# Kernel tuning notes

Measured on AMD Instinct MI355X. Metric: run time of the kernel, lower is better.

## Reference

```python
import jax, jax.numpy as jnp
import numpy as np

B, S, E, H = 2, 2048, 4096, 32
D = E // H  # head_dim = 128
MAX_SEQ = 2048


def precompute_freqs(dim, end, theta=10000.0):
    # Faithful to the torch source, including its operator precedence:
    # freqs = 1.0 / (theta ** arange(0, dim, 2)[:dim//2].float() / dim)
    # i.e. 1.0 / ((theta ** exps) / dim); overflows to inf in fp32 -> freq 0.
    exps = jnp.arange(0, dim, 2, dtype=jnp.float32)[: dim // 2]
    freqs = 1.0 / (jnp.power(jnp.float32(theta), exps) / jnp.float32(dim))
    t = jnp.arange(end, dtype=jnp.float32)
    f = jnp.outer(t, freqs)  # [end, dim//2]
    return jnp.cos(f), jnp.sin(f)


def apply_rope(x, cos, sin, pos):
    # x: [B,H,S,D]; cos/sin: [max_seq, dim//2]; pos: [B,S]
    c = cos[pos][:, None]  # [B,1,S,f]
    s = sin[pos][:, None]
    xr = x.reshape(*x.shape[:-1], -1, 2)  # [B,H,S,D/2,2]
    x1, x2 = xr[..., 0], xr[..., 1]
    if x1.shape[-1] > c.shape[-1]:
        rep = x1.shape[-1] // c.shape[-1]  # repeat_interleave factor
        c = jnp.repeat(c, rep, axis=-1)
        s = jnp.repeat(s, rep, axis=-1)
    out = jnp.stack([x1 * c - x2 * s, x1 * s + x2 * c], axis=-1)
    return out.reshape(x.shape)


def setup_inputs() -> dict:
    key = jax.random.key(0)
    kx, kq, kk, kv, ko = jax.random.split(key, 5)
    x = jax.random.normal(kx, (B, S, E), jnp.float32)
    scale = 0.02
    Wq = jax.random.normal(kq, (E, E), jnp.float32) * scale
    Wk = jax.random.normal(kk, (E, E), jnp.float32) * scale
    Wv = jax.random.normal(kv, (E, E), jnp.float32) * scale
    Wo = jax.random.normal(ko, (E, E), jnp.float32) * scale
    z = jnp.zeros((E,), jnp.float32)
    return {"x": x, "Wq": Wq, "bq": z, "Wk": Wk, "bk": z, "Wv": Wv, "bv": z, "Wo": Wo, "bo": z}


def reference(x, Wq, bq, Wk, bk, Wv, bv, Wo, bo):
    cos, sin = precompute_freqs(H, MAX_SEQ)  # note: dim = n_heads, as in source
    pos = jnp.broadcast_to(jnp.arange(S)[None, :], (B, S))  # no offset, S <= max
    # QKV projections (torch Linear: x @ W.T + b)
    q = (x @ Wq.T + bq).reshape(B, S, H, D).transpose(0, 2, 1, 3)  # [B,H,S,D]
    k = (x @ Wk.T + bk).reshape(B, S, H, D).transpose(0, 2, 1, 3)
    v = (x @ Wv.T + bv).reshape(B, S, H, D).transpose(0, 2, 1, 3)
    q = apply_rope(q, cos, sin, pos)
    k = apply_rope(k, cos, sin, pos)
    # SDPA with mask=None (non-causal, full attention)
    scores = jnp.einsum("bhqd,bhkd->bhqk", q, k) / np.float32(np.sqrt(D))
    att = jax.nn.softmax(scores, axis=-1)
    out = jnp.einsum("bhqk,bhkd->bhqd", att, v)
    out = out.transpose(0, 2, 1, 3).reshape(B, S, E)
    return out @ Wo.T + bo
```

## Files before the change

kernel.cpp:

```cpp
#include <hip/hip_runtime.h>
#include <math.h>

typedef _Float16 half8 __attribute__((ext_vector_type(8)));
typedef _Float16 half4 __attribute__((ext_vector_type(4)));
typedef __fp16 fp16x2 __attribute__((ext_vector_type(2)));
typedef float f32x4 __attribute__((ext_vector_type(4)));
typedef unsigned uint4v __attribute__((ext_vector_type(4)));

struct FreqT { float f[16]; };

__device__ __forceinline__ f32x4 mfma16(half8 a, half8 b, f32x4 c) {
  return __builtin_amdgcn_mfma_f32_16x16x32_f16(a, b, c, 0, 0, 0);
}

__device__ __forceinline__ void gload_lds16(const void* g, void* l) {
  __builtin_amdgcn_global_load_lds(
      (const __attribute__((address_space(1))) void*)g,
      (__attribute__((address_space(3))) void*)l, 16, 0, 0);
}

__device__ __forceinline__ unsigned pk_f16(float p0, float p1) {
  fp16x2 h = __builtin_amdgcn_cvt_pkrtz(p0, p1);
  return __builtin_bit_cast(unsigned, h);
}

#define S_BARRIER() __builtin_amdgcn_s_barrier()
#define WAIT_LGKM0() asm volatile("s_waitcnt lgkmcnt(0)" ::: "memory")
#define WAIT_VM8() asm volatile("s_waitcnt vmcnt(8)" ::: "memory")
#define WAIT_VM4() asm volatile("s_waitcnt vmcnt(4)" ::: "memory")
#define WAIT_VM0() asm volatile("s_waitcnt vmcnt(0)" ::: "memory")

__global__ __launch_bounds__(256)
void cast_f32_f16(const float* __restrict__ in, _Float16* __restrict__ out, long n8) {
  long i = (long)blockIdx.x * blockDim.x + threadIdx.x;
  if (i >= n8) return;
  float4 a = ((const float4*)in)[2 * i];
  float4 b = ((const float4*)in)[2 * i + 1];
  half8 v;
  v[0] = (_Float16)a.x; v[1] = (_Float16)a.y; v[2] = (_Float16)a.z; v[3] = (_Float16)a.w;
  v[4] = (_Float16)b.x; v[5] = (_Float16)b.y; v[6] = (_Float16)b.z; v[7] = (_Float16)b.w;
  ((half8*)out)[i] = v;
}

#define GBM 256
#define GBN 256
#define GBK 64

template <typename OutT>
__global__ __launch_bounds__(512, 2)
void gemm256(const _Float16* __restrict__ A, const _Float16* __restrict__ W,
             const float* __restrict__ bias, OutT* __restrict__ C,
             int M, int N, int K) {
  __shared__ __align__(16) _Float16 lds[4][GBM * GBK];

  int nwg = gridDim.x;
  int bid = blockIdx.x;
  int cpx = nwg >> 3;
  int swz = (bid & 7) * cpx + (bid >> 3);
  int ntn = N / GBN;
  int m0 = (swz / ntn) * GBM, n0 = (swz % ntn) * GBN;

  int tid = threadIdx.x, lane = tid & 63, w = tid >> 6;
  int wm = w >> 2, wn = w & 3;
  int g = lane >> 4, lc = lane & 15;

  int r8 = w * 8 + (lane >> 3);
  int cs = (((lane & 7) ^ (lane >> 3)) << 3);
  const _Float16* gA = A + (size_t)(m0 + r8) * K + cs;
  const _Float16* gB = W + (size_t)(n0 + r8) * K + cs;

#define STAGE(bi, k0) do {                                            \
    _Float16* la_ = &lds[(bi) * 2][0] + w * 512;                      \
    _Float16* lb_ = &lds[(bi) * 2 + 1][0] + w * 512;                  \
    _Pragma("unroll")                                                 \
    for (int i_ = 0; i_ < 4; ++i_) {                                  \
      gload_lds16(gA + (size_t)(i_ * 64) * K + (k0), la_ + i_ * 4096);\
      gload_lds16(gB + (size_t)(i_ * 64) * K + (k0), lb_ + i_ * 4096);\
    } } while (0)

  int aOff[8], bOff[4];
#pragma unroll
  for (int mf = 0; mf < 8; ++mf) aOff[mf] = (wm * 128 + mf * 16 + lc) * 64;
#pragma unroll
  for (int nf = 0; nf < 4; ++nf) bOff[nf] = (wn * 64 + nf * 16 + lc) * 64;
  int co0 = (((0 * 4 + g) ^ (lc & 7)) << 3);
  int co1 = (((1 * 4 + g) ^ (lc & 7)) << 3);

  half8 a0[8], a1[8], b0[4], b1[4];
  f32x4 acc[8][4] = {};

#define LOAD_SET0(bi) do {                                            \
    const _Float16* lA_ = &lds[(bi) * 2][0];                          \
    const _Float16* lB_ = &lds[(bi) * 2 + 1][0];                      \
    _Pragma("unroll")                                                 \
    for (int mf = 0; mf < 4; ++mf) {                                  \
      a0[mf * 2 + 0] = *(const half8*)&lA_[aOff[mf] + co0];           \
      a0[mf * 2 + 1] = *(const half8*)&lA_[aOff[mf] + co1];           \
    }                                                                 \
    _Pragma("unroll")                                                 \
    for (int nf = 0; nf < 2; ++nf) {                                  \
      b0[nf * 2 + 0] = *(const half8*)&lB_[bOff[nf] + co0];           \
      b0[nf * 2 + 1] = *(const half8*)&lB_[bOff[nf] + co1];           \
    } } while (0)

#define LOAD_SET1(bi) do {                                            \
    const _Float16* lA_ = &lds[(bi) * 2][0];                          \
    const _Float16* lB_ = &lds[(bi) * 2 + 1][0];                      \
    _Pragma("unroll")                                                 \
    for (int mf = 0; mf < 4; ++mf) {                                  \
      a1[mf * 2 + 0] = *(const half8*)&lA_[aOff[mf + 4] + co0];       \
      a1[mf * 2 + 1] = *(const half8*)&lA_[aOff[mf + 4] + co1];       \
    }                                                                 \
    _Pragma("unroll")                                                 \
    for (int nf = 0; nf < 2; ++nf) {                                  \
      b1[nf * 2 + 0] = *(const half8*)&lB_[bOff[nf + 2] + co0];       \
      b1[nf * 2 + 1] = *(const half8*)&lB_[bOff[nf + 2] + co1];       \
    } } while (0)

#define MFMA_Q(mq, nq, ar, br) do {                                   \
    __builtin_amdgcn_s_setprio(1);                                    \
    _Pragma("unroll")                                                 \
    for (int mf = 0; mf < 4; ++mf)                                    \
      _Pragma("unroll")                                               \
      for (int nf = 0; nf < 2; ++nf)                                  \
        _Pragma("unroll")                                             \
        for (int kk = 0; kk < 2; ++kk)                                \
          acc[(mq) * 4 + mf][(nq) * 2 + nf] =                         \
              mfma16(ar[mf * 2 + kk], br[nf * 2 + kk],                \
                     acc[(mq) * 4 + mf][(nq) * 2 + nf]);              \
    __builtin_amdgcn_s_setprio(0); } while (0)

  const int NT = K >> 6;

  STAGE(0, 0);
  STAGE(1, GBK);
  WAIT_VM8();
  S_BARRIER();
  LOAD_SET0(0);

  for (int t = 0; t < NT - 2; ++t) {
    int cur = t & 1;
    LOAD_SET1(cur);
    MFMA_Q(0, 0, a0, b0);
    MFMA_Q(0, 1, a0, b1);
    WAIT_LGKM0();
    S_BARRIER();
    STAGE(cur, (t + 2) << 6);
    MFMA_Q(1, 1, a1, b1);
    MFMA_Q(1, 0, a1, b0);
    WAIT_VM8();
    S_BARRIER();
    LOAD_SET0(cur ^ 1);
  }
  {
    int cur = (NT - 2) & 1;
    LOAD_SET1(cur);
    MFMA_Q(0, 0, a0, b0);
    MFMA_Q(0, 1, a0, b1);
    MFMA_Q(1, 1, a1, b1);
    MFMA_Q(1, 0, a1, b0);
    WAIT_VM0();
    S_BARRIER();
    LOAD_SET0(cur ^ 1);
  }
  {
    LOAD_SET1((NT - 1) & 1);
    MFMA_Q(0, 0, a0, b0);
    MFMA_Q(0, 1, a0, b1);
    MFMA_Q(1, 1, a1, b1);
    MFMA_Q(1, 0, a1, b0);
  }

  int crow = m0 + wm * 128 + g * 4;
  int ccol = n0 + wn * 64 + lc;
#pragma unroll
  for (int nf = 0; nf < 4; ++nf) {
    float bv = bias[ccol + nf * 16];
#pragma unroll
    for (int mf = 0; mf < 8; ++mf)
#pragma unroll
      for (int j = 0; j < 4; ++j)
        C[(size_t)(crow + mf * 16 + j) * N + ccol + nf * 16] =
            (OutT)(acc[mf][nf][j] + bv);
  }
#undef STAGE
#undef LOAD_SET0
#undef LOAD_SET1
#undef MFMA_Q
}

__global__ __launch_bounds__(256)
void rope_kernel(_Float16* __restrict__ x, FreqT ft, int Sn, int E, long n8) {
  long i = (long)blockIdx.x * blockDim.x + threadIdx.x;
  if (i >= n8) return;
  int epr = E / 8;
  int e8 = (int)(i % epr);
  int s = (int)((i / epr) % Sn);
  int fj = e8 & 15;
  float fr = ft.f[fj];
  float ang = (float)s * fr;
  float sv, cv;
  sincosf(ang, &sv, &cv);
  half8 v = ((const half8*)x)[i];
  half8 o;
#pragma unroll
  for (int p = 0; p < 4; ++p) {
    float x1 = (float)v[2 * p], x2 = (float)v[2 * p + 1];
    o[2 * p] = (_Float16)(x1 * cv - x2 * sv);
    o[2 * p + 1] = (_Float16)(x1 * sv + x2 * cv);
  }
  ((half8*)x)[i] = o;
}

__global__ __launch_bounds__(256)
void transpose_v(const _Float16* __restrict__ v, _Float16* __restrict__ vt,
                 int Hn, int Sn) {
  const int D = 128;
  const int E = Hn * D;
  __shared__ _Float16 t[64][130];
  int spb = Sn / 64;
  int bid = blockIdx.x;
  int s0 = (bid % spb) * 64;
  int bh = bid / spb;
  int b = bh / Hn, h = bh % Hn;
  int tid = threadIdx.x;
  int r = tid >> 2, dc = (tid & 3) * 32;
  const _Float16* src = v + (size_t)(b * Sn + s0 + r) * E + h * D + dc;
#pragma unroll
  for (int i = 0; i < 4; ++i) {
    half8 x = *(const half8*)(src + i * 8);
#pragma unroll
    for (int k = 0; k < 4; ++k) {
      _Float16 a0 = x[2 * k], a1 = x[2 * k + 1];
      t[r][dc + i * 8 + 2 * k] = a0;
      t[r][dc + i * 8 + 2 * k + 1] = a1;
    }
  }
  __syncthreads();
  int d = tid >> 1, sh = (tid & 1) * 32;
  half8 ov[4];
#pragma unroll
  for (int c = 0; c < 4; ++c)
#pragma unroll
    for (int j = 0; j < 8; ++j)
      ov[c][j] = t[sh + c * 8 + j][d];
  _Float16* dst = vt + ((size_t)bh * D + d) * Sn + s0 + sh;
#pragma unroll
  for (int c = 0; c < 4; ++c)
    *(half8*)(dst + c * 8) = ov[c];
}

#define QB 128
#define KB 64

__global__ __launch_bounds__(256, 3)
void flash_attn(const _Float16* __restrict__ qg, const _Float16* __restrict__ kg,
                const _Float16* __restrict__ vt, _Float16* __restrict__ og,
                int Bn, int Hn, int Sn) {
  const int D = 128;
  const int E = Hn * D;

  __shared__ _Float16 Ksh[2][KB * 128];
  __shared__ _Float16 Vsh[D * KB];
  __shared__ float sm[4][32];

  int qtiles = Sn / QB;
  int bid = blockIdx.x;
  int bh = bid / qtiles, qt = bid % qtiles;
  int b = bh / Hn, h = bh % Hn;

  int tid = threadIdx.x, lane = tid & 63, w = tid >> 6;
  int g = lane >> 4, lc = lane & 15;
  int lc7 = lc & 7;

  const size_t headoff = ((size_t)b * Sn) * E + (size_t)h * D;
  const _Float16* qp = qg + headoff;
  const _Float16* kp = kg + headoff;
  const _Float16* vtp = vt + (size_t)(b * Hn + h) * D * Sn;

  int q0 = qt * QB + w * 32;
  half8 aq[2][4];
#pragma unroll
  for (int mf = 0; mf < 2; ++mf)
#pragma unroll
    for (int kf = 0; kf < 4; ++kf)
      aq[mf][kf] = *(const half8*)(qp + (size_t)(q0 + mf * 16 + lc) * E + kf * 32 + g * 8);

  float mrun[2] = {-1e30f, -1e30f}, lpart[2] = {0.f, 0.f};
  f32x4 o[2][8] = {};

  const float scale = 0.08838834764831845f;

  int krow = 4 * w + (lane >> 4);
  int kcol = ((lane & 15) ^ (krow & 7)) * 8;
  const _Float16* gK = kp + (size_t)krow * E + kcol;
  int vrow = w * 32 + (lane >> 3);
  int vcol = ((lane & 7) ^ (vrow & 7)) * 8;
  const _Float16* gV = vtp + (size_t)vrow * Sn + vcol;

  float* smw = sm[w];

  const int NT = Sn / KB;

  {
    _Float16* lK = Ksh[0] + w * 512;
#pragma unroll
    for (int i = 0; i < 4; ++i)
      gload_lds16(gK + (size_t)(16 * i) * E, lK + i * 2048);
  }
  WAIT_VM0();
  S_BARRIER();

  for (int t = 0; t < NT; ++t) {
    int c = t & 1;
    {
      _Float16* lV = Vsh + w * 2048;
#pragma unroll
      for (int p = 0; p < 4; ++p)
        gload_lds16(gV + (size_t)(p * 8) * Sn + t * KB, lV + p * 512);
    }
    if (t + 1 < NT) {
      _Float16* lK = Ksh[c ^ 1] + w * 512;
#pragma unroll
      for (int i = 0; i < 4; ++i)
        gload_lds16(gK + (size_t)((t + 1) * KB + 16 * i) * E, lK + i * 2048);
    }

    f32x4 st[2][4] = {};
    {
      const _Float16* Kc = Ksh[c];
      __builtin_amdgcn_s_setprio(1);
#pragma unroll
      for (int kf = 0; kf < 4; ++kf) {
        half8 bk[4];
#pragma unroll
        for (int nf = 0; nf < 4; ++nf)
          bk[nf] = *(const half8*)&Kc[(nf * 16 + lc) * 128 + (((kf * 4 + g) ^ lc7) << 3)];
#pragma unroll
        for (int nf = 0; nf < 4; ++nf)
#pragma unroll
          for (int mf = 0; mf < 2; ++mf)
            st[mf][nf] = mfma16(bk[nf], aq[mf][kf], st[mf][nf]);
      }
      __builtin_amdgcn_s_setprio(0);
    }

    bool resc[2];
#pragma unroll
    for (int mf = 0; mf < 2; ++mf) {
      f32x4 m4 = st[mf][0];
#pragma unroll
      for (int nf = 1; nf < 4; ++nf)
#pragma unroll
        for (int j = 0; j < 4; ++j) m4[j] = fmaxf(m4[j], st[mf][nf][j]);
      float mx = fmaxf(fmaxf(m4[0], m4[1]), fmaxf(m4[2], m4[3]));
      mx = fmaxf(mx, __shfl_xor(mx, 16));
      mx = fmaxf(mx, __shfl_xor(mx, 32));
      mx *= scale;
      resc[mf] = __any(mx > mrun[mf] + 8.f);
      if (resc[mf]) {
        float mnew = fmaxf(mrun[mf], mx);
        float r = __expf(mrun[mf] - mnew);
        mrun[mf] = mnew;
        lpart[mf] *= r;
        if (g == 0) smw[mf * 16 + lc] = r;
      }
    }
#pragma unroll
    for (int mf = 0; mf < 2; ++mf)
      if (resc[mf]) {
        f32x4 rv = *(const f32x4*)&smw[mf * 16 + g * 4];
#pragma unroll
        for (int df = 0; df < 8; ++df)
#pragma unroll
          for (int j = 0; j < 4; ++j) o[mf][df][j] *= rv[j];
      }

    half8 pa[2][2];
#pragma unroll
    for (int mf = 0; mf < 2; ++mf) {
      unsigned pk[4][2];
#pragma unroll
      for (int nf = 0; nf < 4; ++nf)
#pragma unroll
        for (int jj = 0; jj < 2; ++jj) {
          float p0 = __expf(st[mf][nf][2 * jj] * scale - mrun[mf]);
          float p1 = __expf(st[mf][nf][2 * jj + 1] * scale - mrun[mf]);
          lpart[mf] += p0 + p1;
          pk[nf][jj] = pk_f16(p0, p1);
        }
#pragma unroll
      for (int kk = 0; kk < 2; ++kk) {
        unsigned A0 = pk[2 * kk][0], B0 = pk[2 * kk + 1][0];
        asm("v_permlane32_swap_b32 %0, %1" : "+v"(A0), "+v"(B0));
        asm("v_permlane16_swap_b32 %0, %1" : "+v"(A0), "+v"(B0));
        unsigned A1 = pk[2 * kk][1], B1 = pk[2 * kk + 1][1];
        asm("v_permlane32_swap_b32 %0, %1" : "+v"(A1), "+v"(B1));
        asm("v_permlane16_swap_b32 %0, %1" : "+v"(A1), "+v"(B1));
        uint4v pv;
        pv[0] = A0; pv[1] = A1; pv[2] = B0; pv[3] = B1;
        pa[mf][kk] = __builtin_bit_cast(half8, pv);
      }
    }

    if (t + 1 < NT) { WAIT_VM4(); } else { WAIT_VM0(); }
    S_BARRIER();

    __builtin_amdgcn_s_setprio(1);
#pragma unroll
    for (int kk = 0; kk < 2; ++kk) {
      int csw = ((kk * 4 + g) ^ lc7) << 3;
#pragma unroll
      for (int df = 0; df < 8; ++df) {
        half8 bv = *(const half8*)&Vsh[(df * 16 + lc) * 64 + csw];
        o[0][df] = mfma16(pa[0][kk], bv, o[0][df]);
        o[1][df] = mfma16(pa[1][kk], bv, o[1][df]);
      }
    }
    __builtin_amdgcn_s_setprio(0);

    if (t + 1 < NT) {
      WAIT_VM0();
      S_BARRIER();
    }
  }

#pragma unroll
  for (int mf = 0; mf < 2; ++mf) {
    float l = lpart[mf];
    l += __shfl_xor(l, 16);
    l += __shfl_xor(l, 32);
    if (g == 0) smw[mf * 16 + lc] = 1.0f / l;
  }
  _Float16* op = og + headoff;
#pragma unroll
  for (int mf = 0; mf < 2; ++mf) {
    f32x4 li = *(const f32x4*)&smw[mf * 16 + g * 4];
#pragma unroll
    for (int j = 0; j < 4; ++j) {
      int row = q0 + mf * 16 + g * 4 + j;
#pragma unroll
      for (int df = 0; df < 8; ++df)
        op[(size_t)row * E + df * 16 + lc] = (_Float16)(o[mf][df][j] * li[j]);
    }
  }
}

extern "C" void kernel_launch(void* const* d_in, const int* in_sizes, int n_in,
                              void* d_out, int out_size, void* d_ws, size_t ws_size,
                              hipStream_t stream) {
  const float* x  = (const float*)d_in[0];
  const float* Wq = (const float*)d_in[1];
  const float* bq = (const float*)d_in[2];
  const float* Wk = (const float*)d_in[3];
  const float* bk = (const float*)d_in[4];
  const float* Wv = (const float*)d_in[5];
  const float* bv = (const float*)d_in[6];
  const float* Wo = (const float*)d_in[7];
  const float* bo = (const float*)d_in[8];

  const int E = in_sizes[2];
  const int M = in_sizes[0] / E;
  const int S = 2048;
  const int Bb = M / S;
  const int H = 32;

  _Float16* xh = (_Float16*)d_ws;
  _Float16* wh = xh + (size_t)M * E;
  _Float16* qh = wh + (size_t)E * E;
  _Float16* kh = qh + (size_t)M * E;
  _Float16* vh = kh + (size_t)M * E;
  _Float16* oh = xh;
  _Float16* vtb = wh;

  FreqT ft;
  for (int j = 0; j < 16; ++j) {
    float pf = (float)pow(10000.0, (double)(2 * j));
    ft.f[j] = 1.0f / (pf / 32.0f);
  }

  long nx8 = (long)M * E / 8;
  long nw8 = (long)E * E / 8;
  dim3 blk(256);
  int cb_x = (int)((nx8 + 255) / 256);
  int cb_w = (int)((nw8 + 255) / 256);
  int gemm_grid = (M / GBM) * (E / GBN);

  cast_f32_f16<<<cb_x, blk, 0, stream>>>(x, xh, nx8);

  cast_f32_f16<<<cb_w, blk, 0, stream>>>(Wq, wh, nw8);
  gemm256<_Float16><<<gemm_grid, 512, 0, stream>>>(xh, wh, bq, qh, M, E, E);
  cast_f32_f16<<<cb_w, blk, 0, stream>>>(Wk, wh, nw8);
  gemm256<_Float16><<<gemm_grid, 512, 0, stream>>>(xh, wh, bk, kh, M, E, E);
  cast_f32_f16<<<cb_w, blk, 0, stream>>>(Wv, wh, nw8);
  gemm256<_Float16><<<gemm_grid, 512, 0, stream>>>(xh, wh, bv, vh, M, E, E);

  rope_kernel<<<cb_x, blk, 0, stream>>>(qh, ft, S, E, nx8);
  rope_kernel<<<cb_x, blk, 0, stream>>>(kh, ft, S, E, nx8);

  transpose_v<<<Bb * H * (S / 64), blk, 0, stream>>>(vh, vtb, H, S);

  flash_attn<<<Bb * H * (S / QB), blk, 0, stream>>>(qh, kh, vtb, oh, Bb, H, S);

  cast_f32_f16<<<cb_w, blk, 0, stream>>>(Wo, wh, nw8);
  gemm256<float><<<gemm_grid, 512, 0, stream>>>(oh, wh, bo, (float*)d_out, M, E, E);
}
```

Measured before the change: 844.4 us.

## Shrink flash-attention query tile to 64 rows and swizzle block order

Halves the query tile per workgroup (each wave now owns 16 query rows instead of 32), which doubles the grid and cuts per-thread registers for the accumulators and scores. It also remaps block IDs with a stride-8 swizzle so consecutive workgroups land on different XCDs or heads. The aim is higher occupancy and better load balance across CUs, at the cost of loading each K/V tile from global memory twice as often per query row.

```diff
diff --git a/kernel.cpp b/kernel.cpp
--- a/kernel.cpp
+++ b/kernel.cpp
@@ -250,7 +250,7 @@
     *(half8*)(dst + c * 8) = ov[c];
 }
 
-#define QB 128
+#define QB 64
 #define KB 64
 
 __global__ __launch_bounds__(256, 3)
@@ -262,11 +262,13 @@
 
   __shared__ _Float16 Ksh[2][KB * 128];
   __shared__ _Float16 Vsh[D * KB];
-  __shared__ float sm[4][32];
+  __shared__ float sm[4][16];
 
   int qtiles = Sn / QB;
+  int nwg = gridDim.x;
   int bid = blockIdx.x;
-  int bh = bid / qtiles, qt = bid % qtiles;
+  int swzb = (bid & 7) * (nwg >> 3) + (bid >> 3);
+  int bh = swzb / qtiles, qt = swzb % qtiles;
   int b = bh / Hn, h = bh % Hn;
 
   int tid = threadIdx.x, lane = tid & 63, w = tid >> 6;
@@ -278,16 +280,15 @@
   const _Float16* kp = kg + headoff;
   const _Float16* vtp = vt + (size_t)(b * Hn + h) * D * Sn;
 
-  int q0 = qt * QB + w * 32;
-  half8 aq[2][4];
-#pragma unroll
-  for (int mf = 0; mf < 2; ++mf)
-#pragma unroll
-    for (int kf = 0; kf < 4; ++kf)
-      aq[mf][kf] = *(const half8*)(qp + (size_t)(q0 + mf * 16 + lc) * E + kf * 32 + g * 8);
-
-  float mrun[2] = {-1e30f, -1e30f}, lpart[2] = {0.f, 0.f};
-  f32x4 o[2][8] = {};
+  int q0 = qt * QB + w * 16;
+  half8 aq0, aq1, aq2, aq3;
+  aq0 = *(const half8*)(qp + (size_t)(q0 + lc) * E + 0 * 32 + g * 8);
+  aq1 = *(const half8*)(qp + (size_t)(q0 + lc) * E + 1 * 32 + g * 8);
+  aq2 = *(const half8*)(qp + (size_t)(q0 + lc) * E + 2 * 32 + g * 8);
+  aq3 = *(const half8*)(qp + (size_t)(q0 + lc) * E + 3 * 32 + g * 8);
+
+  float mrun = -1e30f, lpart = 0.f;
+  f32x4 o[8] = {};
 
   const float scale = 0.08838834764831845f;
 
@@ -326,95 +327,107 @@
         gload_lds16(gK + (size_t)((t + 1) * KB + 16 * i) * E, lK + i * 2048);
     }
 
-    f32x4 st[2][4] = {};
+    f32x4 st[4] = {};
     {
       const _Float16* Kc = Ksh[c];
       __builtin_amdgcn_s_setprio(1);
 #pragma unroll
       for (int kf = 0; kf < 4; ++kf) {
-        half8 bk[4];
-#pragma unroll
-        for (int nf = 0; nf < 4; ++nf)
-          bk[nf] = *(const half8*)&Kc[(nf * 16 + lc) * 128 + (((kf * 4 + g) ^ lc7) << 3)];
-#pragma unroll
-        for (int nf = 0; nf < 4; ++nf)
-#pragma unroll
-          for (int mf = 0; mf < 2; ++mf)
-            st[mf][nf] = mfma16(bk[nf], aq[mf][kf], st[mf][nf]);
+        half8 aqk = (kf == 0) ? aq0 : (kf == 1) ? aq1 : (kf == 2) ? aq2 : aq3;
+#pragma unroll
+        for (int nf = 0; nf < 4; ++nf) {
+          half8 bk = *(const half8*)&Kc[(nf * 16 + lc) * 128 + (((kf * 4 + g) ^ lc7) << 3)];
+          st[nf] = mfma16(bk, aqk, st[nf]);
+        }
       }
       __builtin_amdgcn_s_setprio(0);
     }
 
-    bool resc[2];
-#pragma unroll
-    for (int mf = 0; mf < 2; ++mf) {
-      f32x4 m4 = st[mf][0];
+    {
+      f32x4 m4 = st[0];
 #pragma unroll
       for (int nf = 1; nf < 4; ++nf)
 #pragma unroll
-        for (int j = 0; j < 4; ++j) m4[j] = fmaxf(m4[j], st[mf][nf][j]);
+        for (int j = 0; j < 4; ++j) m4[j] = fmaxf(m4[j], st[nf][j]);
       float mx = fmaxf(fmaxf(m4[0], m4[1]), fmaxf(m4[2], m4[3]));
       mx = fmaxf(mx, __shfl_xor(mx, 16));
       mx = fmaxf(mx, __shfl_xor(mx, 32));
       mx *= scale;
-      resc[mf] = __any(mx > mrun[mf] + 8.f);
-      if (resc[mf]) {
-        float mnew = fmaxf(mrun[mf], mx);
-        float r = __expf(mrun[mf] - mnew);
-        mrun[mf] = mnew;
-        lpart[mf] *= r;
-        if (g == 0) smw[mf * 16 + lc] = r;
+      bool resc = __any(mx > mrun + 8.f);
+      if (resc) {
+        float mnew = fmaxf(mrun, mx);
+        float r = __expf(mrun - mnew);
+        mrun = mnew;
+        lpart *= r;
+        if (g == 0) smw[lc] = r;
       }
-    }
-#pragma unroll
-    for (int mf = 0; mf < 2; ++mf)
-      if (resc[mf]) {
-        f32x4 rv = *(const f32x4*)&smw[mf * 16 + g * 4];
+      if (resc) {
+        f32x4 rv = *(const f32x4*)&smw[g * 4];
 #pragma unroll
         for (int df = 0; df < 8; ++df)
 #pragma unroll
-          for (int j = 0; j < 4; ++j) o[mf][df][j] *= rv[j];
+          for (int j = 0; j < 4; ++j) o[df][j] *= rv[j];
       }
-
-    half8 pa[2][2];
-#pragma unroll
-    for (int mf = 0; mf < 2; ++mf) {
-      unsigned pk[4][2];
-#pragma unroll
-      for (int nf = 0; nf < 4; ++nf)
-#pragma unroll
-        for (int jj = 0; jj < 2; ++jj) {
-          float p0 = __expf(st[mf][nf][2 * jj] * scale - mrun[mf]);
-          float p1 = __expf(st[mf][nf][2 * jj + 1] * scale - mrun[mf]);
-          lpart[mf] += p0 + p1;
-          pk[nf][jj] = pk_f16(p0, p1);
-        }
-#pragma unroll
-      for (int kk = 0; kk < 2; ++kk) {
-        unsigned A0 = pk[2 * kk][0], B0 = pk[2 * kk + 1][0];
-        asm("v_permlane32_swap_b32 %0, %1" : "+v"(A0), "+v"(B0));
-        asm("v_permlane16_swap_b32 %0, %1" : "+v"(A0), "+v"(B0));
-        unsigned A1 = pk[2 * kk][1], B1 = pk[2 * kk + 1][1];
-        asm("v_permlane32_swap_b32 %0, %1" : "+v"(A1), "+v"(B1));
-        asm("v_permlane16_swap_b32 %0, %1" : "+v"(A1), "+v"(B1));
-        uint4v pv;
-        pv[0] = A0; pv[1] = A1; pv[2] = B0; pv[3] = B1;
-        pa[mf][kk] = __builtin_bit_cast(half8, pv);
-      }
+    }
+
+    half8 pa0, pa1;
+    {
+      float e0, e1;
+      e0 = __expf(st[0][0] * scale - mrun);
+      e1 = __expf(st[0][1] * scale - mrun);
+      lpart += e0 + e1; unsigned k00 = pk_f16(e0, e1);
+      e0 = __expf(st[0][2] * scale - mrun);
+      e1 = __expf(st[0][3] * scale - mrun);
+      lpart += e0 + e1; unsigned k01 = pk_f16(e0, e1);
+      e0 = __expf(st[1][0] * scale - mrun);
+      e1 = __expf(st[1][1] * scale - mrun);
+      lpart += e0 + e1; unsigned k10 = pk_f16(e0, e1);
+      e0 = __expf(st[1][2] * scale - mrun);
+      e1 = __expf(st[1][3] * scale - mrun);
+      lpart += e0 + e1; unsigned k11 = pk_f16(e0, e1);
+      e0 = __expf(st[2][0] * scale - mrun);
+      e1 = __expf(st[2][1] * scale - mrun);
+      lpart += e0 + e1; unsigned k20 = pk_f16(e0, e1);
+      e0 = __expf(st[2][2] * scale - mrun);
+      e1 = __expf(st[2][3] * scale - mrun);
+      lpart += e0 + e1; unsigned k21 = pk_f16(e0, e1);
+      e0 = __expf(st[3][0] * scale - mrun);
+      e1 = __expf(st[3][1] * scale - mrun);
+      lpart += e0 + e1; unsigned k30 = pk_f16(e0, e1);
+      e0 = __expf(st[3][2] * scale - mrun);
+      e1 = __expf(st[3][3] * scale - mrun);
+      lpart += e0 + e1; unsigned k31 = pk_f16(e0, e1);
+      asm("v_permlane32_swap_b32 %0, %1" : "+v"(k00), "+v"(k10));
+      asm("v_permlane16_swap_b32 %0, %1" : "+v"(k00), "+v"(k10));
+      asm("v_permlane32_swap_b32 %0, %1" : "+v"(k01), "+v"(k11));
+      asm("v_permlane16_swap_b32 %0, %1" : "+v"(k01), "+v"(k11));
+      asm("v_permlane32_swap_b32 %0, %1" : "+v"(k20), "+v"(k30));
+      asm("v_permlane16_swap_b32 %0, %1" : "+v"(k20), "+v"(k30));
+      asm("v_permlane32_swap_b32 %0, %1" : "+v"(k21), "+v"(k31));
+      asm("v_permlane16_swap_b32 %0, %1" : "+v"(k21), "+v"(k31));
+      uint4v p0v, p1v;
+      p0v[0] = k00; p0v[1] = k01; p0v[2] = k10; p0v[3] = k11;
+      p1v[0] = k20; p1v[1] = k21; p1v[2] = k30; p1v[3] = k31;
+      pa0 = __builtin_bit_cast(half8, p0v);
+      pa1 = __builtin_bit_cast(half8, p1v);
     }
 
     if (t + 1 < NT) { WAIT_VM4(); } else { WAIT_VM0(); }
     S_BARRIER();
 
     __builtin_amdgcn_s_setprio(1);
-#pragma unroll
-    for (int kk = 0; kk < 2; ++kk) {
-      int csw = ((kk * 4 + g) ^ lc7) << 3;
+    {
+      int csw0 = (g ^ lc7) << 3;
+      int csw1 = ((4 + g) ^ lc7) << 3;
 #pragma unroll
       for (int df = 0; df < 8; ++df) {
-        half8 bv = *(const half8*)&Vsh[(df * 16 + lc) * 64 + csw];
-        o[0][df] = mfma16(pa[0][kk], bv, o[0][df]);
-        o[1][df] = mfma16(pa[1][kk], bv, o[1][df]);
+        half8 bv0 = *(const half8*)&Vsh[(df * 16 + lc) * 64 + csw0];
+        o[df] = mfma16(pa0, bv0, o[df]);
+      }
+#pragma unroll
+      for (int df = 0; df < 8; ++df) {
+        half8 bv1 = *(const half8*)&Vsh[(df * 16 + lc) * 64 + csw1];
+        o[df] = mfma16(pa1, bv1, o[df]);
       }
     }
     __builtin_amdgcn_s_setprio(0);
@@ -425,23 +438,21 @@
     }
   }
 
-#pragma unroll
-  for (int mf = 0; mf < 2; ++mf) {
-    float l = lpart[mf];
+  {
+    float l = lpart;
     l += __shfl_xor(l, 16);
     l += __shfl_xor(l, 32);
-    if (g == 0) smw[mf * 16 + lc] = 1.0f / l;
+    if (g == 0) smw[lc] = 1.0f / l;
   }
   _Float16* op = og + headoff;
-#pragma unroll
-  for (int mf = 0; mf < 2; ++mf) {
-    f32x4 li = *(const f32x4*)&smw[mf * 16 + g * 4];
+  {
+    f32x4 li = *(const f32x4*)&smw[g * 4];
 #pragma unroll
     for (int j = 0; j < 4; ++j) {
-      int row = q0 + mf * 16 + g * 4 + j;
+      int row = q0 + g * 4 + j;
 #pragma unroll
       for (int df = 0; df < 8; ++df)
-        op[(size_t)row * E + df * 16 + lc] = (_Float16)(o[mf][df][j] * li[j]);
+        op[(size_t)row * E + df * 16 + lc] = (_Float16)(o[df][j] * li[j]);
     }
   }
 }
```

After: 793.3 us. 1.06x faster.
